# Optimization experiments

Hardware: AMD Instinct MI355X
Metric: run time of the kernel (lower is better)

The kernel has to match this reference:

```python
import jax, jax.numpy as jnp
import numpy as np

B, D, C = 512, 16384, 3
SAMPLE_DURATION = 16
NEG_THRESHOLD = 0.5
NEGPOS_RATIO = 3


def setup_inputs() -> dict:
    key = jax.random.key(0)
    k1, k2, k3, k4, k5, k6, k7 = jax.random.split(key, 7)
    loc_pred = jax.random.normal(k1, (B, D, 2), dtype=jnp.float32)
    conf_pred = jax.random.normal(k2, (B, D, C), dtype=jnp.float32)
    # one ground-truth (start, end, label) per sample, within [0, 16]
    start = jax.random.uniform(k3, (B,), dtype=jnp.float32) * 8.0
    length = 1.0 + jax.random.uniform(k4, (B,), dtype=jnp.float32) * 7.0
    label = jax.random.randint(k5, (B,), 0, C).astype(jnp.float32)
    targets = jnp.stack([start, start + length, label], axis=-1)  # [B,3]
    # default bars stored as (center, length) in frame units
    centers = 1.0 + jax.random.uniform(k6, (D,), dtype=jnp.float32) * (SAMPLE_DURATION - 2.0)
    lengths = 1.0 + jax.random.uniform(k7, (D,), dtype=jnp.float32) * (SAMPLE_DURATION - 4.0)
    default_bar = jnp.stack([centers, lengths], axis=-1)  # [D,2]
    return {"loc_pred": loc_pred, "conf_pred": conf_pred,
            "targets": targets, "default_bar": default_bar}


def _match_one(truth, label, default):
    """truth [2]=(start,end), label scalar int, default [D,2]=(center,length).
    Returns loc_t [D,2], conf_t [D] (0=ignore, 1=background, >1=fg)."""
    d_c, d_l = default[:, 0], default[:, 1]
    d_s, d_e = d_c - d_l * 0.5, d_c + d_l * 0.5
    inter = jnp.clip(jnp.minimum(truth[1], d_e) - jnp.maximum(truth[0], d_s), 0.0)
    union = (truth[1] - truth[0]) + (d_e - d_s) - inter
    ov = inter / union                                   # [D] 1-D IoU
    best_prior = jnp.argmax(ov)                          # best anchor for the truth
    bto = ov.at[best_prior].set(2.0)                     # index_fill_ with 2
    conf = jnp.full((D,), label + 1, dtype=jnp.int32)    # single truth -> broadcast
    is_bg = conf == 1
    conf = jnp.where(bto < NEG_THRESHOLD, 0, conf)
    conf = jnp.where(is_bg, 1, conf)
    # SSD-style encoding of matched (start,end) against (center,length)
    m_c = (truth[0] + truth[1]) * 0.5
    m_l = truth[1] - truth[0]
    loc = jnp.stack([(m_c - d_c) / d_l, jnp.log(m_l / d_l)], axis=-1)  # [D,2]
    return loc, conf


def reference(loc_pred, conf_pred, targets, default_bar):
    truths = targets[:, :2]                              # [B,2]
    labels = targets[:, 2].astype(jnp.int32)             # [B]
    loc_t, conf_t = jax.vmap(_match_one, in_axes=(0, 0, None))(truths, labels, default_bar)
    loc_t = jax.lax.stop_gradient(loc_t)                 # built under no_grad in torch
    conf_t = jax.lax.stop_gradient(conf_t)

    pos = conf_t > 0                                     # [B,D] used for mining
    loc_pos = conf_t > 1                                 # [B,D] used for loc loss

    # SmoothL1 (beta=1), reduction='sum' over positives
    diff = loc_pred - loc_t
    ad = jnp.abs(diff)
    sl1 = jnp.where(ad < 1.0, 0.5 * diff * diff, ad - 0.5)
    loss_loc = jnp.sum(sl1 * loc_pos[..., None].astype(sl1.dtype))

    # hard-negative mining on per-anchor CE surrogate
    conf_tc = jnp.clip(conf_t - 1, 0)                    # [B,D] class ids 0..C-1
    lse = jax.nn.logsumexp(conf_pred, axis=-1)           # [B,D]
    gathered = jnp.take_along_axis(conf_pred, conf_tc[..., None], axis=-1)[..., 0]
    lc = lse - gathered
    lc = jnp.where(pos, 0.0, lc)
    loss_idx = jnp.argsort(-lc, axis=1)                  # descending sort
    idx_rank = jnp.argsort(loss_idx, axis=1)
    num_pos = jnp.sum(pos.astype(jnp.int32), axis=1, keepdims=True)   # [B,1]
    num_neg = jnp.clip(NEGPOS_RATIO * num_pos, max=D - 1)
    neg = idx_rank < num_neg                             # [B,D]

    sel = (pos | neg).astype(conf_pred.dtype)
    logp = jax.nn.log_softmax(conf_pred, axis=-1)
    ce = -jnp.take_along_axis(logp, conf_tc[..., None], axis=-1)[..., 0]
    loss_conf = jnp.sum(ce * sel)

    N = jnp.sum(num_pos).astype(loss_loc.dtype)
    return jnp.stack([loss_loc / N, loss_conf / N])
```

## Files before the change

kernel.cpp:

```cpp
#include <hip/hip_runtime.h>
#include <hip/hip_fp16.h>
#include <math.h>

constexpr int Bn = 512;
constexpr int Dn = 16384;
constexpr int BS = 512;
constexpr int CHUNKS = 16;
constexpr int CPRI = Dn / CHUNKS;
constexpr int K1T = 256;

__device__ __forceinline__ float lse3(float a, float b, float c) {
  float m = fmaxf(a, fmaxf(b, c));
  return m + __logf(__expf(a - m) + __expf(b - m) + __expf(c - m));
}
__device__ __forceinline__ float sl1f(float x) {
  float a = fabsf(x);
  return a < 1.f ? 0.5f * x * x : a - 0.5f;
}

__device__ __forceinline__ double blockReduceAddD(double v, double* sred) {
  int t = threadIdx.x;
  sred[t] = v;
  __syncthreads();
  for (int off = BS >> 1; off > 0; off >>= 1) {
    if (t < off) sred[t] += sred[t + off];
    __syncthreads();
  }
  double r = sred[0];
  __syncthreads();
  return r;
}

__global__ __launch_bounds__(K1T) void multiloss_stream(
    const float* __restrict__ loc_pred, const float* __restrict__ conf_pred,
    const float* __restrict__ targets, const float* __restrict__ default_bar,
    unsigned short* __restrict__ lc16,
    float* __restrict__ pce, float* __restrict__ plloc, int* __restrict__ pnpos,
    float* __restrict__ pbv, int* __restrict__ pbi)
{
  __shared__ float s_conf[CPRI * 3];
  __shared__ float s_bar[CPRI * 2];

  const int bid = blockIdx.x;
  const int b = bid >> 4, c = bid & 15;
  const int t = threadIdx.x;
  const int wbase = t & ~63;

  {
    const float4* srcC = (const float4*)(conf_pred + (size_t)b * Dn * 3) + (size_t)c * (CPRI * 3 / 4);
    float4* dstC = (float4*)s_conf;
    #pragma unroll
    for (int j = 0; j < 3; ++j)
      __builtin_amdgcn_global_load_lds(
          (const __attribute__((address_space(1))) void*)(srcC + j * 256 + t),
          (__attribute__((address_space(3))) void*)(dstC + j * 256 + wbase), 16, 0, 0);
    const float4* srcB = (const float4*)default_bar + (size_t)c * (CPRI * 2 / 4);
    float4* dstB = (float4*)s_bar;
    #pragma unroll
    for (int j = 0; j < 2; ++j)
      __builtin_amdgcn_global_load_lds(
          (const __attribute__((address_space(1))) void*)(srcB + j * 256 + t),
          (__attribute__((address_space(3))) void*)(dstB + j * 256 + wbase), 16, 0, 0);
  }

  const float t0  = targets[b * 3 + 0];
  const float t1  = targets[b * 3 + 1];
  const int   lab = (int)targets[b * 3 + 2];

  float ce = 0.f, lloc = 0.f; int npos = 0;
  float bInter = -1.f, bUni = 1.f; int bestI = 0;
  const float m_c = (t0 + t1) * 0.5f;
  const float m_l = t1 - t0;

  __syncthreads();

  if (lab == 0) {
    #pragma unroll
    for (int i = 0; i < CPRI / K1T; ++i) {
      int p = i * K1T + t;
      float c0 = s_conf[3 * p], c1 = s_conf[3 * p + 1], c2 = s_conf[3 * p + 2];
      ce += lse3(c0, c1, c2) - c0;
    }
  } else {
    unsigned short* __restrict__ lcrow = lc16 + (size_t)b * Dn + (size_t)c * CPRI;
    #pragma unroll
    for (int i = 0; i < CPRI / K1T; ++i) {
      int p = i * K1T + t;
      float c0 = s_conf[3 * p], c1 = s_conf[3 * p + 1], c2 = s_conf[3 * p + 2];
      float2 db = ((const float2*)s_bar)[p];
      float d_c = db.x, d_l = db.y;
      float d_s = d_c - d_l * 0.5f;
      float d_e = d_c + d_l * 0.5f;
      float inter = fmaxf(fminf(t1, d_e) - fmaxf(t0, d_s), 0.f);
      float uni = (t1 - t0) + (d_e - d_s) - inter;
      const int g = c * CPRI + p;
      float lhs = inter * bUni, rhs = bInter * uni;
      if (lhs > rhs || (lhs == rhs && g < bestI)) { bInter = inter; bUni = uni; bestI = g; }
      float lcv = (2.f * inter >= uni) ? 0.f : (lse3(c0, c1, c2) - c0);
      lcrow[p] = __half_as_ushort(__float2half(lcv));
    }
    const float log_ml = __logf(m_l);
    const float2* __restrict__ lp2 = (const float2*)loc_pred + (size_t)b * Dn + (size_t)c * CPRI;
    #pragma unroll
    for (int i = 0; i < CPRI / K1T; ++i) {
      int p = i * K1T + t;
      float2 db = ((const float2*)s_bar)[p];
      float d_c = db.x, d_l = db.y;
      float d_s = d_c - d_l * 0.5f;
      float d_e = d_c + d_l * 0.5f;
      float inter = fmaxf(fminf(t1, d_e) - fmaxf(t0, d_s), 0.f);
      float uni = (t1 - t0) + (d_e - d_s) - inter;
      if (2.f * inter >= uni) {
        npos++;
        float c0 = s_conf[3 * p], c1 = s_conf[3 * p + 1], c2 = s_conf[3 * p + 2];
        float lse = lse3(c0, c1, c2);
        float cl = (lab == 1) ? c1 : c2;
        ce += lse - cl;
        float2 lp = lp2[p];
        float pd0 = lp.x - __fdividef(m_c - d_c, d_l);
        float pd1 = (lp.y - log_ml) + __logf(d_l);
        lloc += sl1f(pd0) + sl1f(pd1);
      }
    }
  }

  #pragma unroll
  for (int off = 1; off < 64; off <<= 1) {
    ce   += __shfl_xor(ce, off);
    lloc += __shfl_xor(lloc, off);
    npos += __shfl_xor(npos, off);
    float oI = __shfl_xor(bInter, off);
    float oU = __shfl_xor(bUni, off);
    int   oX = __shfl_xor(bestI, off);
    float lhs = oI * bUni, rhs = bInter * oU;
    if (lhs > rhs || (lhs == rhs && oX < bestI)) { bInter = oI; bUni = oU; bestI = oX; }
  }
  __syncthreads();
  float* red = s_bar;
  if ((t & 63) == 0) {
    int w = t >> 6;
    red[w * 6 + 0] = ce; red[w * 6 + 1] = lloc; red[w * 6 + 2] = __int_as_float(npos);
    red[w * 6 + 3] = bInter; red[w * 6 + 4] = bUni; red[w * 6 + 5] = __int_as_float(bestI);
  }
  __syncthreads();
  if (t == 0) {
    float Ce = red[0], Ll = red[1]; int Np = __float_as_int(red[2]);
    float Bi = red[3], Bu = red[4]; int Bx = __float_as_int(red[5]);
    for (int k = 1; k < 4; ++k) {
      Ce += red[k * 6 + 0]; Ll += red[k * 6 + 1]; Np += __float_as_int(red[k * 6 + 2]);
      float oI = red[k * 6 + 3], oU = red[k * 6 + 4]; int oX = __float_as_int(red[k * 6 + 5]);
      float lhs = oI * Bu, rhs = Bi * oU;
      if (lhs > rhs || (lhs == rhs && oX < Bx)) { Bi = oI; Bu = oU; Bx = oX; }
    }
    int pidx = b * CHUNKS + c;
    pce[pidx] = Ce; plloc[pidx] = Ll; pnpos[pidx] = Np;
    pbv[pidx] = Bi / Bu;
    pbi[pidx] = Bx;
  }
}

__global__ __launch_bounds__(BS) void multiloss_select(
    const float* __restrict__ loc_pred, const float* __restrict__ conf_pred,
    const float* __restrict__ targets, const float* __restrict__ default_bar,
    const unsigned short* __restrict__ lc16,
    const float* __restrict__ pce, const float* __restrict__ plloc,
    const int* __restrict__ pnpos, const float* __restrict__ pbv, const int* __restrict__ pbi,
    double* __restrict__ rloc, double* __restrict__ rconf, double* __restrict__ rnp)
{
  __shared__ unsigned short s_lc[Dn];
  __shared__ int      s_hist[256];
  __shared__ double   s_dred[BS];
  __shared__ unsigned s_wt[8];
  __shared__ unsigned s_sel[2];
  __shared__ double   s_sc[2];
  __shared__ int      s_np;

  const int b = blockIdx.x;
  const int t = threadIdx.x;
  const int lab = (int)targets[b * 3 + 2];

  if (lab == 0) {
    if (t == 0) {
      double ce = 0.0;
      for (int kk = 0; kk < CHUNKS; ++kk) ce += (double)pce[CHUNKS * b + kk];
      rloc[b] = 0.0; rconf[b] = ce; rnp[b] = (double)Dn;
    }
    return;
  }

  const float4* lcr = (const float4*)(lc16 + (size_t)b * Dn);
  float4* sl4 = (float4*)s_lc;
  #pragma unroll
  for (int j = 0; j < Dn / 8 / BS; ++j) sl4[j * BS + t] = lcr[j * BS + t];
  __syncthreads();

  if (t == 0) {
    const float t0 = targets[b * 3 + 0];
    const float t1 = targets[b * 3 + 1];
    double ce = 0.0, ll = 0.0; int np = 0;
    float bV = -1.f; int bI = 0;
    for (int kk = 0; kk < CHUNKS; ++kk) {
      int pi = CHUNKS * b + kk;
      ce += (double)pce[pi]; ll += (double)plloc[pi]; np += pnpos[pi];
      float v = pbv[pi]; int i2 = pbi[pi];
      if (v > bV || (v == bV && i2 < bI)) { bV = v; bI = i2; }
    }
    if (bV < 0.5f) {
      int d = bI;
      const float* cp = conf_pred + (size_t)b * Dn * 3 + (size_t)d * 3;
      float c0 = cp[0], c1 = cp[1], c2 = cp[2];
      float lse = lse3(c0, c1, c2);
      float cl = (lab == 1) ? c1 : c2;
      ce += (double)(lse - cl);
      float2 db = ((const float2*)default_bar)[d];
      float2 lp = ((const float2*)loc_pred)[(size_t)b * Dn + d];
      float m_c = (t0 + t1) * 0.5f, m_l = t1 - t0;
      float pd0 = lp.x - (m_c - db.x) / db.y;
      float pd1 = lp.y - __logf(m_l / db.y);
      ll += (double)(sl1f(pd0) + sl1f(pd1));
      np += 1;
      s_lc[d] = 0;
    }
    s_sc[0] = ce; s_sc[1] = ll; s_np = np;
  }
  __syncthreads();
  const int np = s_np;
  const int k = min(3 * np, Dn - 1);

  unsigned prefix = 0;
  int K = k;
  const int lane = t & 63, w = t >> 6;
  for (int r = 0; r < 2; ++r) {
    if (t < 256) s_hist[t] = 0;
    __syncthreads();
    for (int d = t; d < Dn; d += BS) {
      unsigned u = s_lc[d];
      bool ok = (r == 0) || ((u >> 8) == prefix);
      if (ok) {
        unsigned bin = (r == 0) ? (u >> 8) : (u & 0xFFu);
        atomicAdd(&s_hist[bin], 1);
      }
    }
    __syncthreads();
    unsigned psum = (t < 256) ? (unsigned)s_hist[t] : 0u;
    unsigned incl = psum;
    #pragma unroll
    for (int off = 1; off < 64; off <<= 1) {
      unsigned v = __shfl_down(incl, off, 64);
      if (lane + off < 64) incl += v;
    }
    if (lane == 0) s_wt[w] = incl;
    __syncthreads();
    unsigned aboveW = 0;
    for (int w2 = w + 1; w2 < 8; ++w2) aboveW += s_wt[w2];
    const unsigned above = aboveW + (incl - psum);
    if (t < 256 && above < (unsigned)K && (unsigned)K <= above + psum) {
      s_sel[0] = (unsigned)t;
      s_sel[1] = above;
    }
    __syncthreads();
    unsigned selBin = s_sel[0];
    K -= (int)s_sel[1];
    prefix = (r == 0) ? selBin : ((prefix << 8) | selBin);
    __syncthreads();
  }
  const unsigned tb = prefix;

  float    ssum = 0.f;
  unsigned scnt = 0;
  for (int d = t; d < Dn; d += BS) {
    unsigned u = s_lc[d];
    if (u > tb) {
      ssum += __half2float(__ushort_as_half((unsigned short)u));
      scnt++;
    }
  }
  double S = blockReduceAddD((double)ssum, s_dred);
  double C = blockReduceAddD((double)scnt, s_dred);

  if (t == 0) {
    double tval = (double)__half2float(__ushort_as_half((unsigned short)tb));
    double topk = S + ((double)k - C) * tval;
    rloc[b]  = s_sc[1];
    rconf[b] = s_sc[0] + topk;
    rnp[b]   = (double)np;
  }
}

__global__ __launch_bounds__(BS) void multiloss_mono(
    const float* __restrict__ loc_pred, const float* __restrict__ conf_pred,
    const float* __restrict__ targets, const float* __restrict__ default_bar,
    double* __restrict__ rloc, double* __restrict__ rconf, double* __restrict__ rnp)
{
  __shared__ float    s_lc[Dn];
  __shared__ int      s_hist[2048];
  __shared__ unsigned s_scan[BS];
  __shared__ double   s_dred[BS];
  __shared__ unsigned s_sel[2];
  __shared__ double   s_corr[2];
  __shared__ int      s_np;

  const int b = blockIdx.x;
  const int t = threadIdx.x;

  const float t0  = targets[b * 3 + 0];
  const float t1  = targets[b * 3 + 1];
  const int   lab = (int)targets[b * 3 + 2];

  const float* __restrict__ cpb = conf_pred + (size_t)b * Dn * 3;

  if (lab == 0) {
    float ce = 0.f;
    for (int d = t; d < Dn; d += BS) {
      const float* cp = cpb + d * 3;
      ce += lse3(cp[0], cp[1], cp[2]) - cp[0];
    }
    double tot = blockReduceAddD((double)ce, s_dred);
    if (t == 0) { rloc[b] = 0.0; rconf[b] = tot; rnp[b] = (double)Dn; }
    return;
  }

  const float m_c = (t0 + t1) * 0.5f;
  const float m_l = t1 - t0;

  float bestV = -1.f; int bestI = 0;
  int   nposL = 0;
  float cePosL = 0.f;
  float llocL  = 0.f;

  for (int d = t; d < Dn; d += BS) {
    float2 db = ((const float2*)default_bar)[d];
    float d_c = db.x, d_l = db.y;
    float d_s = d_c - d_l * 0.5f;
    float d_e = d_c + d_l * 0.5f;
    float inter = fmaxf(fminf(t1, d_e) - fmaxf(t0, d_s), 0.f);
    float uni = (t1 - t0) + (d_e - d_s) - inter;
    float ov  = inter / uni;

    const float* cp = cpb + d * 3;
    float c0 = cp[0];
    float lse = lse3(cp[0], cp[1], cp[2]);

    if (ov > bestV) { bestV = ov; bestI = d; }

    float lcv;
    if (ov >= 0.5f) {
      nposL++;
      float cl = (lab == 1) ? cp[1] : cp[2];
      cePosL += lse - cl;
      float2 lp = ((const float2*)loc_pred)[(size_t)b * Dn + d];
      float pd0 = lp.x - (m_c - d_c) / d_l;
      float pd1 = lp.y - __logf(m_l / d_l);
      llocL += sl1f(pd0) + sl1f(pd1);
      lcv = 0.f;
    } else {
      lcv = lse - c0;
    }
    s_lc[d] = lcv;
  }

  float* sv = (float*)s_hist;
  int*   si = (int*)(s_hist + BS);
  sv[t] = bestV; si[t] = bestI;
  __syncthreads();
  for (int off = BS >> 1; off > 0; off >>= 1) {
    if (t < off) {
      float v2 = sv[t + off]; int i2 = si[t + off];
      if (v2 > sv[t] || (v2 == sv[t] && i2 < si[t])) { sv[t] = v2; si[t] = i2; }
    }
    __syncthreads();
  }
  float bV = sv[0]; int bI = si[0];
  __syncthreads();

  double nposTot  = blockReduceAddD((double)nposL, s_dred);
  double cePosTot = blockReduceAddD((double)cePosL, s_dred);
  double llocTot  = blockReduceAddD((double)llocL, s_dred);
  int num_pos = (int)(nposTot + 0.5);

  if (t == 0) {
    double cc = 0.0, lcor = 0.0; int np2 = num_pos;
    if (bV < 0.5f) {
      int d = bI;
      const float* cp = cpb + d * 3;
      float lse = lse3(cp[0], cp[1], cp[2]);
      float cl = (lab == 1) ? cp[1] : cp[2];
      cc = (double)(lse - cl);
      float2 db = ((const float2*)default_bar)[d];
      float2 lp = ((const float2*)loc_pred)[(size_t)b * Dn + d];
      float pd0 = lp.x - (m_c - db.x) / db.y;
      float pd1 = lp.y - __logf(m_l / db.y);
      lcor = (double)(sl1f(pd0) + sl1f(pd1));
      np2 += 1;
      s_lc[d] = 0.f;
    }
    s_corr[0] = cc; s_corr[1] = lcor; s_np = np2;
  }
  __syncthreads();
  int np = s_np;
  int k  = min(3 * np, Dn - 1);

  unsigned prefix = 0;
  int K = k;
  for (int r = 0; r < 3; ++r) {
    for (int i = t; i < 2048; i += BS) s_hist[i] = 0;
    __syncthreads();
    for (int d = t; d < Dn; d += BS) {
      unsigned u = __float_as_uint(s_lc[d]);
      bool ok = (r == 0) || (r == 1 ? ((u >> 21) == prefix) : ((u >> 10) == prefix));
      if (ok) {
        unsigned bin = (r == 0) ? (u >> 21)
                     : (r == 1) ? ((u >> 10) & 0x7FFu)
                                : (u & 0x3FFu);
        atomicAdd(&s_hist[bin], 1);
      }
    }
    __syncthreads();
    int nb  = (r == 2) ? 1024 : 2048;
    int per = nb / BS;
    unsigned psum = 0;
    for (int j = 0; j < per; ++j) psum += (unsigned)s_hist[t * per + j];
    s_scan[t] = psum;
    __syncthreads();
    for (int off = 1; off < BS; off <<= 1) {
      unsigned v = (t + off < BS) ? s_scan[t + off] : 0u;
      __syncthreads();
      s_scan[t] += v;
      __syncthreads();
    }
    unsigned above = (t < BS - 1) ? s_scan[t + 1] : 0u;
    if (above < (unsigned)K && (unsigned)K <= above + psum) {
      unsigned cum = above;
      int found = 0;
      for (int j = per - 1; j >= 0; --j) {
        unsigned c = (unsigned)s_hist[t * per + j];
        if (cum + c >= (unsigned)K) { found = j; break; }
        cum += c;
      }
      s_sel[0] = (unsigned)(t * per + found);
      s_sel[1] = cum;
    }
    __syncthreads();
    unsigned selBin = s_sel[0];
    K -= (int)s_sel[1];
    prefix = (r == 0) ? selBin
           : (r == 1) ? ((prefix << 11) | selBin)
                      : ((prefix << 10) | selBin);
    __syncthreads();
  }
  const unsigned tb = prefix;

  float    ssum = 0.f;
  unsigned scnt = 0;
  for (int d = t; d < Dn; d += BS) {
    float v = s_lc[d];
    if (__float_as_uint(v) > tb) { ssum += v; scnt++; }
  }
  double S = blockReduceAddD((double)ssum, s_dred);
  double C = blockReduceAddD((double)scnt, s_dred);

  if (t == 0) {
    double tval = (double)__uint_as_float(tb);
    double topk = S + ((double)k - C) * tval;
    rloc[b]  = llocTot + s_corr[1];
    rconf[b] = cePosTot + s_corr[0] + topk;
    rnp[b]   = (double)s_np;
  }
}

__global__ __launch_bounds__(512) void multiloss_final(
    const double* __restrict__ rloc, const double* __restrict__ rconf,
    const double* __restrict__ rnp, float* __restrict__ out)
{
  __shared__ double s1[512], s2[512], s3[512];
  int t = threadIdx.x;
  s1[t] = rloc[t];
  s2[t] = rconf[t];
  s3[t] = rnp[t];
  __syncthreads();
  for (int off = 256; off > 0; off >>= 1) {
    if (t < off) { s1[t] += s1[t + off]; s2[t] += s2[t + off]; s3[t] += s3[t + off]; }
    __syncthreads();
  }
  if (t == 0) {
    double N = s3[0];
    out[0] = (float)(s1[0] / N);
    out[1] = (float)(s2[0] / N);
  }
}

extern "C" void kernel_launch(void* const* d_in, const int* in_sizes, int n_in,
                              void* d_out, int out_size, void* d_ws, size_t ws_size,
                              hipStream_t stream) {
  const float* loc_pred    = (const float*)d_in[0];
  const float* conf_pred   = (const float*)d_in[1];
  const float* targets     = (const float*)d_in[2];
  const float* default_bar = (const float*)d_in[3];
  float* out = (float*)d_out;
  char* ws = (char*)d_ws;

  constexpr size_t LC_BYTES = (size_t)Bn * Dn * sizeof(unsigned short);
  constexpr size_t P_CNT = (size_t)Bn * CHUNKS;
  size_t off = LC_BYTES;
  float*  pce   = (float*)(ws + off); off += P_CNT * 4;
  float*  plloc = (float*)(ws + off); off += P_CNT * 4;
  int*    pnpos = (int*)(ws + off);   off += P_CNT * 4;
  float*  pbv   = (float*)(ws + off); off += P_CNT * 4;
  int*    pbi   = (int*)(ws + off);   off += P_CNT * 4;
  double* rloc  = (double*)(ws + off); off += Bn * 8;
  double* rconf = (double*)(ws + off); off += Bn * 8;
  double* rnp   = (double*)(ws + off); off += Bn * 8;
  const size_t NEED = off;

  if (ws_size >= NEED) {
    hipLaunchKernelGGL(multiloss_stream, dim3(Bn * CHUNKS), dim3(K1T), 0, stream,
                       loc_pred, conf_pred, targets, default_bar,
                       (unsigned short*)ws, pce, plloc, pnpos, pbv, pbi);
    hipLaunchKernelGGL(multiloss_select, dim3(Bn), dim3(BS), 0, stream,
                       loc_pred, conf_pred, targets, default_bar,
                       (const unsigned short*)ws, pce, plloc, pnpos, pbv, pbi,
                       rloc, rconf, rnp);
    hipLaunchKernelGGL(multiloss_final, dim3(1), dim3(512), 0, stream,
                       rloc, rconf, rnp, out);
  } else {
    double* mloc  = (double*)ws;
    double* mconf = mloc + Bn;
    double* mnp   = mconf + Bn;
    hipLaunchKernelGGL(multiloss_mono, dim3(Bn), dim3(BS), 0, stream,
                       loc_pred, conf_pred, targets, default_bar, mloc, mconf, mnp);
    hipLaunchKernelGGL(multiloss_final, dim3(1), dim3(512), 0, stream,
                       mloc, mconf, mnp, out);
  }
}
```

Measured before the change: 65.20 us.

## Defer best-prior argmax to fallback path and compact positives per wave

The stream kernel no longer tracks the per-chunk best IoU anchor. That argmax is now recomputed in the select kernel only when a row has zero positives. Positives are compacted into a per-wave shared list via ballot/mbcnt, so the loc-loss pass touches only positive anchors instead of recomputing IoU for all. The kernel also grows to 512 threads per block with single-pass LDS loads, and reuses one logsumexp for both the CE and the negative-loss value. This cuts ALU work, shuffles and partial-result traffic, at the cost of a rare slower fallback scan over the default bars.

After: 62.05 us. 1.05x faster.

```diff
diff --git a/kernel.cpp b/kernel.cpp
--- a/kernel.cpp
+++ b/kernel.cpp
@@ -7,7 +7,7 @@
 constexpr int BS = 512;
 constexpr int CHUNKS = 16;
 constexpr int CPRI = Dn / CHUNKS;
-constexpr int K1T = 256;
+constexpr int K1T = 512;
 
 __device__ __forceinline__ float lse3(float a, float b, float c) {
   float m = fmaxf(a, fmaxf(b, c));
@@ -35,32 +35,34 @@
     const float* __restrict__ loc_pred, const float* __restrict__ conf_pred,
     const float* __restrict__ targets, const float* __restrict__ default_bar,
     unsigned short* __restrict__ lc16,
-    float* __restrict__ pce, float* __restrict__ plloc, int* __restrict__ pnpos,
-    float* __restrict__ pbv, int* __restrict__ pbi)
+    float* __restrict__ pce, float* __restrict__ plloc, int* __restrict__ pnpos)
 {
   __shared__ float s_conf[CPRI * 3];
   __shared__ float s_bar[CPRI * 2];
+  __shared__ unsigned short s_plist[CPRI];
+  __shared__ float s_red[24];
 
   const int bid = blockIdx.x;
   const int b = bid >> 4, c = bid & 15;
   const int t = threadIdx.x;
-  const int wbase = t & ~63;
+  const int l = t & 63, w = t >> 6;
+  const int wb = t & ~63;
 
   {
-    const float4* srcC = (const float4*)(conf_pred + (size_t)b * Dn * 3) + (size_t)c * (CPRI * 3 / 4);
+    const float4* srcC = (const float4*)(conf_pred + (size_t)b * Dn * 3) + (size_t)c * 768;
     float4* dstC = (float4*)s_conf;
-    #pragma unroll
-    for (int j = 0; j < 3; ++j)
+    __builtin_amdgcn_global_load_lds(
+        (const __attribute__((address_space(1))) void*)(srcC + t),
+        (__attribute__((address_space(3))) void*)(dstC + wb), 16, 0, 0);
+    if (t < 256)
       __builtin_amdgcn_global_load_lds(
-          (const __attribute__((address_space(1))) void*)(srcC + j * 256 + t),
-          (__attribute__((address_space(3))) void*)(dstC + j * 256 + wbase), 16, 0, 0);
-    const float4* srcB = (const float4*)default_bar + (size_t)c * (CPRI * 2 / 4);
+          (const __attribute__((address_space(1))) void*)(srcC + 512 + t),
+          (__attribute__((address_space(3))) void*)(dstC + 512 + wb), 16, 0, 0);
+    const float4* srcB = (const float4*)default_bar + (size_t)c * 512;
     float4* dstB = (float4*)s_bar;
-    #pragma unroll
-    for (int j = 0; j < 2; ++j)
-      __builtin_amdgcn_global_load_lds(
-          (const __attribute__((address_space(1))) void*)(srcB + j * 256 + t),
-          (__attribute__((address_space(3))) void*)(dstB + j * 256 + wbase), 16, 0, 0);
+    __builtin_amdgcn_global_load_lds(
+        (const __attribute__((address_space(1))) void*)(srcB + t),
+        (__attribute__((address_space(3))) void*)(dstB + wb), 16, 0, 0);
   }
 
   const float t0  = targets[b * 3 + 0];
@@ -68,9 +70,9 @@
   const int   lab = (int)targets[b * 3 + 2];
 
   float ce = 0.f, lloc = 0.f; int npos = 0;
-  float bInter = -1.f, bUni = 1.f; int bestI = 0;
   const float m_c = (t0 + t1) * 0.5f;
   const float m_l = t1 - t0;
+  const float T   = t1 - t0;
 
   __syncthreads();
 
@@ -79,48 +81,52 @@
     for (int i = 0; i < CPRI / K1T; ++i) {
       int p = i * K1T + t;
       float c0 = s_conf[3 * p], c1 = s_conf[3 * p + 1], c2 = s_conf[3 * p + 2];
-      ce += lse3(c0, c1, c2) - c0;
+      float hi = fmaxf(c0, c1), lo = fminf(c0, c1);
+      float m  = fmaxf(hi, c2), mid = fminf(hi, c2);
+      float s  = 1.f + __expf(lo - m) + __expf(mid - m);
+      ce += (m - c0) + __logf(s);
     }
   } else {
     unsigned short* __restrict__ lcrow = lc16 + (size_t)b * Dn + (size_t)c * CPRI;
+    unsigned wcnt = 0;
+    unsigned short* plist = s_plist + (w << 7);
     #pragma unroll
-    for (int i = 0; i < CPRI / K1T; ++i) {
-      int p = i * K1T + t;
+    for (int i = 0; i < 2; ++i) {
+      const int p = (w << 7) + (i << 6) + l;
       float c0 = s_conf[3 * p], c1 = s_conf[3 * p + 1], c2 = s_conf[3 * p + 2];
       float2 db = ((const float2*)s_bar)[p];
       float d_c = db.x, d_l = db.y;
-      float d_s = d_c - d_l * 0.5f;
-      float d_e = d_c + d_l * 0.5f;
+      float d_s = __fmaf_rn(-0.5f, d_l, d_c);
+      float d_e = __fmaf_rn(0.5f, d_l, d_c);
       float inter = fmaxf(fminf(t1, d_e) - fmaxf(t0, d_s), 0.f);
-      float uni = (t1 - t0) + (d_e - d_s) - inter;
-      const int g = c * CPRI + p;
-      float lhs = inter * bUni, rhs = bInter * uni;
-      if (lhs > rhs || (lhs == rhs && g < bestI)) { bInter = inter; bUni = uni; bestI = g; }
-      float lcv = (2.f * inter >= uni) ? 0.f : (lse3(c0, c1, c2) - c0);
+      float uni = (T + d_l) - inter;
+      bool pos = (2.f * inter >= uni);
+      npos += pos;
+      float hi = fmaxf(c0, c1), lo = fminf(c0, c1);
+      float m  = fmaxf(hi, c2), mid = fminf(hi, c2);
+      float s  = 1.f + __expf(lo - m) + __expf(mid - m);
+      float lnS = __logf(s);
+      float cl = (lab == 1) ? c1 : c2;
+      ce += pos ? ((m - cl) + lnS) : 0.f;
+      float lcv = pos ? 0.f : ((m - c0) + lnS);
       lcrow[p] = __half_as_ushort(__float2half(lcv));
+      unsigned long long mask = __ballot(pos);
+      if (pos) {
+        unsigned off = __builtin_amdgcn_mbcnt_hi((unsigned)(mask >> 32),
+                       __builtin_amdgcn_mbcnt_lo((unsigned)mask, 0u));
+        plist[wcnt + off] = (unsigned short)p;
+      }
+      wcnt += (unsigned)__popcll(mask);
     }
     const float log_ml = __logf(m_l);
     const float2* __restrict__ lp2 = (const float2*)loc_pred + (size_t)b * Dn + (size_t)c * CPRI;
-    #pragma unroll
-    for (int i = 0; i < CPRI / K1T; ++i) {
-      int p = i * K1T + t;
+    for (unsigned j = l; j < wcnt; j += 64) {
+      int p = plist[j];
       float2 db = ((const float2*)s_bar)[p];
-      float d_c = db.x, d_l = db.y;
-      float d_s = d_c - d_l * 0.5f;
-      float d_e = d_c + d_l * 0.5f;
-      float inter = fmaxf(fminf(t1, d_e) - fmaxf(t0, d_s), 0.f);
-      float uni = (t1 - t0) + (d_e - d_s) - inter;
-      if (2.f * inter >= uni) {
-        npos++;
-        float c0 = s_conf[3 * p], c1 = s_conf[3 * p + 1], c2 = s_conf[3 * p + 2];
-        float lse = lse3(c0, c1, c2);
-        float cl = (lab == 1) ? c1 : c2;
-        ce += lse - cl;
-        float2 lp = lp2[p];
-        float pd0 = lp.x - __fdividef(m_c - d_c, d_l);
-        float pd1 = (lp.y - log_ml) + __logf(d_l);
-        lloc += sl1f(pd0) + sl1f(pd1);
-      }
+      float2 lp = lp2[p];
+      float pd0 = lp.x - __fdividef(m_c - db.x, db.y);
+      float pd1 = (lp.y - log_ml) + __logf(db.y);
+      lloc += sl1f(pd0) + sl1f(pd1);
     }
   }
 
@@ -129,33 +135,19 @@
     ce   += __shfl_xor(ce, off);
     lloc += __shfl_xor(lloc, off);
     npos += __shfl_xor(npos, off);
-    float oI = __shfl_xor(bInter, off);
-    float oU = __shfl_xor(bUni, off);
-    int   oX = __shfl_xor(bestI, off);
-    float lhs = oI * bUni, rhs = bInter * oU;
-    if (lhs > rhs || (lhs == rhs && oX < bestI)) { bInter = oI; bUni = oU; bestI = oX; }
-  }
-  __syncthreads();
-  float* red = s_bar;
-  if ((t & 63) == 0) {
-    int w = t >> 6;
-    red[w * 6 + 0] = ce; red[w * 6 + 1] = lloc; red[w * 6 + 2] = __int_as_float(npos);
-    red[w * 6 + 3] = bInter; red[w * 6 + 4] = bUni; red[w * 6 + 5] = __int_as_float(bestI);
+  }
+  if (l == 0) {
+    s_red[w * 3 + 0] = ce; s_red[w * 3 + 1] = lloc; s_red[w * 3 + 2] = __int_as_float(npos);
   }
   __syncthreads();
   if (t == 0) {
-    float Ce = red[0], Ll = red[1]; int Np = __float_as_int(red[2]);
-    float Bi = red[3], Bu = red[4]; int Bx = __float_as_int(red[5]);
-    for (int k = 1; k < 4; ++k) {
-      Ce += red[k * 6 + 0]; Ll += red[k * 6 + 1]; Np += __float_as_int(red[k * 6 + 2]);
-      float oI = red[k * 6 + 3], oU = red[k * 6 + 4]; int oX = __float_as_int(red[k * 6 + 5]);
-      float lhs = oI * Bu, rhs = Bi * oU;
-      if (lhs > rhs || (lhs == rhs && oX < Bx)) { Bi = oI; Bu = oU; Bx = oX; }
+    float Ce = 0.f, Ll = 0.f; int Np = 0;
+    #pragma unroll
+    for (int k = 0; k < 8; ++k) {
+      Ce += s_red[k * 3 + 0]; Ll += s_red[k * 3 + 1]; Np += __float_as_int(s_red[k * 3 + 2]);
     }
     int pidx = b * CHUNKS + c;
     pce[pidx] = Ce; plloc[pidx] = Ll; pnpos[pidx] = Np;
-    pbv[pidx] = Bi / Bu;
-    pbi[pidx] = Bx;
   }
 }
 
@@ -164,12 +156,14 @@
     const float* __restrict__ targets, const float* __restrict__ default_bar,
     const unsigned short* __restrict__ lc16,
     const float* __restrict__ pce, const float* __restrict__ plloc,
-    const int* __restrict__ pnpos, const float* __restrict__ pbv, const int* __restrict__ pbi,
+    const int* __restrict__ pnpos,
     double* __restrict__ rloc, double* __restrict__ rconf, double* __restrict__ rnp)
 {
   __shared__ unsigned short s_lc[Dn];
   __shared__ int      s_hist[256];
   __shared__ double   s_dred[BS];
+  __shared__ float    s_fv[BS];
+  __shared__ int      s_fi[BS];
   __shared__ unsigned s_wt[8];
   __shared__ unsigned s_sel[2];
   __shared__ double   s_sc[2];
@@ -188,6 +182,9 @@
     return;
   }
 
+  const float t0 = targets[b * 3 + 0];
+  const float t1 = targets[b * 3 + 1];
+
   const float4* lcr = (const float4*)(lc16 + (size_t)b * Dn);
   float4* sl4 = (float4*)s_lc;
   #pragma unroll
@@ -195,36 +192,55 @@
   __syncthreads();
 
   if (t == 0) {
-    const float t0 = targets[b * 3 + 0];
-    const float t1 = targets[b * 3 + 1];
     double ce = 0.0, ll = 0.0; int np = 0;
-    float bV = -1.f; int bI = 0;
     for (int kk = 0; kk < CHUNKS; ++kk) {
       int pi = CHUNKS * b + kk;
       ce += (double)pce[pi]; ll += (double)plloc[pi]; np += pnpos[pi];
-      float v = pbv[pi]; int i2 = pbi[pi];
-      if (v > bV || (v == bV && i2 < bI)) { bV = v; bI = i2; }
-    }
-    if (bV < 0.5f) {
-      int d = bI;
+    }
+    s_sc[0] = ce; s_sc[1] = ll; s_np = np;
+  }
+  __syncthreads();
+  int np = s_np;
+
+  if (np == 0) {
+    float bV = -1.f; int bI = 0;
+    for (int d = t; d < Dn; d += BS) {
+      float2 db = ((const float2*)default_bar)[d];
+      float d_s = db.x - db.y * 0.5f;
+      float d_e = db.x + db.y * 0.5f;
+      float inter = fmaxf(fminf(t1, d_e) - fmaxf(t0, d_s), 0.f);
+      float uni = (t1 - t0) + (d_e - d_s) - inter;
+      float ov = inter / uni;
+      if (ov > bV) { bV = ov; bI = d; }
+    }
+    s_fv[t] = bV; s_fi[t] = bI;
+    __syncthreads();
+    for (int off = BS >> 1; off > 0; off >>= 1) {
+      if (t < off) {
+        float v2 = s_fv[t + off]; int i2 = s_fi[t + off];
+        if (v2 > s_fv[t] || (v2 == s_fv[t] && i2 < s_fi[t])) { s_fv[t] = v2; s_fi[t] = i2; }
+      }
+      __syncthreads();
+    }
+    if (t == 0) {
+      int d = s_fi[0];
       const float* cp = conf_pred + (size_t)b * Dn * 3 + (size_t)d * 3;
       float c0 = cp[0], c1 = cp[1], c2 = cp[2];
       float lse = lse3(c0, c1, c2);
       float cl = (lab == 1) ? c1 : c2;
-      ce += (double)(lse - cl);
       float2 db = ((const float2*)default_bar)[d];
       float2 lp = ((const float2*)loc_pred)[(size_t)b * Dn + d];
       float m_c = (t0 + t1) * 0.5f, m_l = t1 - t0;
       float pd0 = lp.x - (m_c - db.x) / db.y;
       float pd1 = lp.y - __logf(m_l / db.y);
-      ll += (double)(sl1f(pd0) + sl1f(pd1));
-      np += 1;
+      s_sc[0] += (double)(lse - cl);
+      s_sc[1] += (double)(sl1f(pd0) + sl1f(pd1));
+      s_np = 1;
       s_lc[d] = 0;
     }
-    s_sc[0] = ce; s_sc[1] = ll; s_np = np;
-  }
-  __syncthreads();
-  const int np = s_np;
+    __syncthreads();
+    np = s_np;
+  }
   const int k = min(3 * np, Dn - 1);
 
   unsigned prefix = 0;
@@ -505,8 +521,6 @@
   float*  pce   = (float*)(ws + off); off += P_CNT * 4;
   float*  plloc = (float*)(ws + off); off += P_CNT * 4;
   int*    pnpos = (int*)(ws + off);   off += P_CNT * 4;
-  float*  pbv   = (float*)(ws + off); off += P_CNT * 4;
-  int*    pbi   = (int*)(ws + off);   off += P_CNT * 4;
   double* rloc  = (double*)(ws + off); off += Bn * 8;
   double* rconf = (double*)(ws + off); off += Bn * 8;
   double* rnp   = (double*)(ws + off); off += Bn * 8;
@@ -515,10 +529,10 @@
   if (ws_size >= NEED) {
     hipLaunchKernelGGL(multiloss_stream, dim3(Bn * CHUNKS), dim3(K1T), 0, stream,
                        loc_pred, conf_pred, targets, default_bar,
-                       (unsigned short*)ws, pce, plloc, pnpos, pbv, pbi);
+                       (unsigned short*)ws, pce, plloc, pnpos);
     hipLaunchKernelGGL(multiloss_select, dim3(Bn), dim3(BS), 0, stream,
                        loc_pred, conf_pred, targets, default_bar,
-                       (const unsigned short*)ws, pce, plloc, pnpos, pbv, pbi,
+                       (const unsigned short*)ws, pce, plloc, pnpos,
                        rloc, rconf, rnp);
     hipLaunchKernelGGL(multiloss_final, dim3(1), dim3(512), 0, stream,
                        rloc, rconf, rnp, out);
```
